# Optimization experiments

Hardware: AMD Instinct MI355X
Metric: run time of the kernel (lower is better)

The kernel has to match this reference:

```python
import jax, jax.numpy as jnp
import numpy as np

T, N, F, H = 64, 20000, 8, 32
E = 320000
NEG_SLOPE = 0.01  # torch.nn.LeakyReLU default


def setup_inputs() -> dict:
    key = jax.random.key(0)
    ks = jax.random.split(key, 16)
    g = lambda k, shape, fan_in: jax.random.normal(k, shape, jnp.float32) * (1.0 / np.sqrt(fan_in))
    return {
        "x": jax.random.normal(ks[0], (T, N, F), jnp.float32),
        "edge_index": jax.random.randint(ks[1], (2, E), 0, N, jnp.int64),
        "edge_weight": jax.random.uniform(ks[2], (E,), jnp.float32),
        "h": jnp.zeros((N, H), jnp.float32),
        # GConvGRU(K=1): each ChebConv reduces to a dense Linear (only T_0 = X term)
        "Wxz": g(ks[3], (F, H), F), "bxz": jnp.zeros((H,), jnp.float32),
        "Whz": g(ks[4], (H, H), H), "bhz": jnp.zeros((H,), jnp.float32),
        "Wxr": g(ks[5], (F, H), F), "bxr": jnp.zeros((H,), jnp.float32),
        "Whr": g(ks[6], (H, H), H), "bhr": jnp.zeros((H,), jnp.float32),
        "Wxh": g(ks[7], (F, H), F), "bxh": jnp.zeros((H,), jnp.float32),
        "Whh": g(ks[8], (H, H), H), "bhh": jnp.zeros((H,), jnp.float32),
        "W1": g(ks[9], (H, 1), H), "b1": jnp.zeros((1,), jnp.float32),
        "W2": g(ks[10], (N, 1), N), "b2": jnp.zeros((1,), jnp.float32),
    }


def reference(x, edge_index, edge_weight, h,
              Wxz, bxz, Whz, bhz, Wxr, bxr, Whr, bhr, Wxh, bxh, Whh, bhh,
              W1, b1, W2, b2):
    # GConvGRU with Chebyshev order K=1: each ChebConv is out = X @ W + b
    # (edge_index / edge_weight only participate for K >= 2, faithful to source).
    def gru_step(hc, xt):  # hc: [N,H], xt: [N,F]
        z = jax.nn.sigmoid(xt @ Wxz + bxz + hc @ Whz + bhz)
        r = jax.nn.sigmoid(xt @ Wxr + bxr + hc @ Whr + bhr)
        h_tilde = jnp.tanh(xt @ Wxh + bxh + (hc * r) @ Whh + bhh)
        hn = z * hc + (1.0 - z) * h_tilde
        return hn, hn

    h_fin, h_tensor = jax.lax.scan(gru_step, h, x)  # h_tensor: [T,N,H]
    a = jax.nn.leaky_relu(h_tensor, NEG_SLOPE)       # LeakyReLU(h_tensor)
    a = jax.nn.leaky_relu(a @ W1 + b1, NEG_SLOPE)    # linear1 -> [T,N,1], then LeakyReLU
    a = a[..., 0]                                    # squeeze -> [T,N]
    out = (a @ W2 + b2)[..., 0]                      # linear2 -> [T,1] -> squeeze -> [T]
    return (out, h_fin)
```

## Files before the change

kernel.cpp:

```cpp
#include <hip/hip_runtime.h>
#include <hip/hip_bf16.h>

#define T_STEPS 64
#define N_NODES 20000
#define F_IN    8
#define H_DIM   32
#define NEG_SLOPE 0.01f
#define WS_STRIDE 32
#define LOG2E 1.44269504f

typedef __attribute__((ext_vector_type(8))) short bf16x8;
typedef __attribute__((ext_vector_type(4))) float f32x4;

#define MFMA(a, b, c) __builtin_amdgcn_mfma_f32_16x16x32_bf16((a), (b), (c), 0, 0, 0)

__device__ __forceinline__ unsigned short f2bf(float f) {
    unsigned u = __float_as_uint(f);
    u += 0x7FFFu + ((u >> 16) & 1u);
    return (unsigned short)(u >> 16);
}
__device__ __forceinline__ float bf2f(unsigned short s) {
    return __uint_as_float(((unsigned)s) << 16);
}
__device__ __forceinline__ void split_pack8_rne(const float* v, bf16x8& hi, bf16x8& lo) {
    union { unsigned u[4]; bf16x8 v8; } H, L;
#pragma unroll
    for (int p = 0; p < 4; ++p) {
        float a = v[2*p], b = v[2*p+1];
        unsigned short ha = f2bf(a), hb = f2bf(b);
        unsigned short la = f2bf(a - bf2f(ha)), lb = f2bf(b - bf2f(hb));
        H.u[p] = (unsigned)ha | ((unsigned)hb << 16);
        L.u[p] = (unsigned)la | ((unsigned)lb << 16);
    }
    hi = H.v8; lo = L.v8;
}

__device__ __forceinline__ unsigned cvtpk(float a, float b) {
    union { __hip_bfloat162 h; unsigned u; } U;
    U.h = __float22bfloat162_rn(float2{a, b});
    return U.u;
}


__device__ __forceinline__ void load_wfragW(const float* __restrict__ W, int c, int q,
                                            int Rout, int Rown, int Roth, float scale,
                                            bf16x8& hi, bf16x8& lo) {
    float v[8];
#pragma unroll
    for (int j = 0; j < 8; ++j) {
        int dim = (j < 4) ? (Rown + 4*q + j) : (Roth + 4*q + (j - 4));
        v[j] = W[dim * H_DIM + (Rout + c)] * scale;
    }
    split_pack8_rne(v, hi, lo);
}

__device__ __forceinline__ bf16x8 load_xwfragW(const float* __restrict__ Wx,
                                               const float* __restrict__ bx,
                                               const float* __restrict__ bh,
                                               int c, int q, int Rout, float scale) {
    union { unsigned short s[8]; bf16x8 v8; } U;
#pragma unroll
    for (int j = 0; j < 8; ++j) U.s[j] = 0;
    if (q == 0) {
#pragma unroll
        for (int j = 0; j < 8; ++j) U.s[j] = f2bf(Wx[j * H_DIM + Rout + c] * scale);
    } else if (q == 1) {
#pragma unroll
        for (int j = 0; j < 8; ++j) {
            float w0 = Wx[j * H_DIM + Rout + c] * scale;
            unsigned short h = f2bf(w0);
            U.s[j] = f2bf(w0 - bf2f(h));
        }
    } else if (q == 3) {
        float b = (bx[Rout + c] + bh[Rout + c]) * scale;
        unsigned short h = f2bf(b);
        U.s[0] = h;
        U.s[1] = f2bf(b - bf2f(h));
    }
    return U.v8;
}

__device__ __forceinline__ bf16x8 build_xbfrag2(const float* v, int q) {
    union { unsigned u[4]; bf16x8 v8; } U;
#pragma unroll
    for (int p = 0; p < 4; ++p) {
        unsigned val = cvtpk(v[2*p], v[2*p+1]);
        if (q == 2) val = 0u;
        if (q == 3) val = (p == 0) ? 0x3F803F80u : 0u;
        U.u[p] = val;
    }
    return U.v8;
}

__device__ __forceinline__ bf16x8 frag_own(unsigned w01, unsigned w23) {
    union { unsigned u[4]; bf16x8 v8; } U;
    U.u[0] = w01; U.u[1] = w23; U.u[2] = 0u; U.u[3] = 0u;
    return U.v8;
}
__device__ __forceinline__ bf16x8 frag_peer(unsigned w01, unsigned w23) {
    union { unsigned u[4]; bf16x8 v8; } U;
    U.u[0] = 0u; U.u[1] = 0u; U.u[2] = w01; U.u[3] = w23;
    return U.v8;
}

__device__ __forceinline__ float sigmoid2_f(float xp) {
    return __builtin_amdgcn_rcpf(1.0f + __builtin_amdgcn_exp2f(-xp));
}
__device__ __forceinline__ float tanh2_f(float yp) {
    return 1.0f - 2.0f * __builtin_amdgcn_rcpf(1.0f + __builtin_amdgcn_exp2f(yp));
}
__device__ __forceinline__ float leaky_f(float x) {
    return fmaxf(x, NEG_SLOPE * x);
}

__global__ void final_kernel(const float* __restrict__ ws, const float* __restrict__ b2,
                             float* __restrict__ out) {
    int t = threadIdx.x;
    if (t < T_STEPS) out[t] = ws[t * WS_STRIDE] + b2[0];
}

__global__ __launch_bounds__(128, 3) void rgcn_mfma_kernel(
    const float* __restrict__ x,
    const float* __restrict__ h0,
    const float* __restrict__ Wxz, const float* __restrict__ bxz,
    const float* __restrict__ Whz, const float* __restrict__ bhz,
    const float* __restrict__ Wxr, const float* __restrict__ bxr,
    const float* __restrict__ Whr, const float* __restrict__ bhr,
    const float* __restrict__ Wxh, const float* __restrict__ bxh,
    const float* __restrict__ Whh, const float* __restrict__ bhh,
    const float* __restrict__ W1,  const float* __restrict__ b1,
    const float* __restrict__ W2,
    float* __restrict__ ws,
    float* __restrict__ out)
{
    const int tid  = threadIdx.x;
    const int w    = tid >> 6;
    const int l    = tid & 63;
    const int c    = l & 15;
    const int q    = l >> 4;
    const int base = blockIdx.x * 16;
    const int node = base + c;
    const int Rown = 16 * w;
    const int Roth = 16 - Rown;

    __shared__ __align__(8) uint2 hxbuf[2][2][4][16];
    __shared__ __align__(8) uint2 rhbuf[2][4][16];
    __shared__ unsigned short pbuf16[T_STEPS][130];

    bf16x8 WHrOh, WHrOl, WHzh, WHzl, WHhh, WHhl;
    load_wfragW(Whr, c, q, Rown, Rown, Roth, LOG2E,        WHrOh, WHrOl);
    load_wfragW(Whz, c, q, Rown, Rown, Roth, LOG2E,        WHzh,  WHzl);
    load_wfragW(Whh, c, q, Rown, Rown, Roth, 2.0f * LOG2E, WHhh,  WHhl);
    bf16x8 WXrO = load_xwfragW(Wxr, bxr, bhr, c, q, Rown, LOG2E);
    bf16x8 WXz  = load_xwfragW(Wxz, bxz, bhz, c, q, Rown, LOG2E);
    bf16x8 WXh  = load_xwfragW(Wxh, bxh, bhh, c, q, Rown, 2.0f * LOG2E);

    float w1v[4];
#pragma unroll
    for (int i = 0; i < 4; ++i) w1v[i] = W1[Rown + 4*q + i];
    const float b1s = b1[0];
    const float w2l = W2[node];

    float hv[4];
    unsigned own01, own23;
    {
        float4 h4 = ((const float4*)(h0 + (size_t)node * H_DIM + Rown))[q];
        hv[0] = h4.x; hv[1] = h4.y; hv[2] = h4.z; hv[3] = h4.w;
        own01 = cvtpk(hv[0], hv[1]);
        own23 = cvtpk(hv[2], hv[3]);
        hxbuf[0][w][q][c] = uint2{own01, own23};
    }

    const f32x4 zero4 = {0.0f, 0.0f, 0.0f, 0.0f};

    f32x4 axrO, axz, axh;
    {
        const float4* xp = (const float4*)(x + (size_t)node * F_IN);
        float4 x0 = xp[0], x1 = xp[1];
        float xv[8] = {x0.x, x0.y, x0.z, x0.w, x1.x, x1.y, x1.z, x1.w};
        bf16x8 fx0 = build_xbfrag2(xv, q);
        axrO = MFMA(WXrO, fx0, zero4);
        axz  = MFMA(WXz,  fx0, zero4);
        axh  = MFMA(WXh,  fx0, zero4);
    }
    float4 cx0, cx1;
    {
        const float4* xp = (const float4*)(x + (size_t)(N_NODES * F_IN)
                                             + (size_t)node * F_IN);
        cx0 = xp[0]; cx1 = xp[1];
    }

    __syncthreads();

#pragma unroll 1
    for (int t = 0; t < T_STEPS; ++t) {
        const int rp = t & 1;

        uint2 ohp = hxbuf[rp][1 - w][q][c];

        bf16x8 fhO = frag_own(own01, own23);
        f32x4 arA = MFMA(WHrOh, fhO, axrO);
        f32x4 arB = MFMA(WHrOl, fhO, zero4);
        f32x4 azA = MFMA(WHzh,  fhO, axz);
        f32x4 azB = MFMA(WHzl,  fhO, zero4);

        int tt = (t + 2 < T_STEPS) ? (t + 2) : (T_STEPS - 1);
        const float4* xp = (const float4*)(x + (size_t)tt * (N_NODES * F_IN)
                                             + (size_t)node * F_IN);
        float4 nx0 = xp[0], nx1 = xp[1];

        bf16x8 fhP = frag_peer(ohp.x, ohp.y);
        arA = MFMA(WHrOh, fhP, arA);
        arB = MFMA(WHrOl, fhP, arB);
        azA = MFMA(WHzh,  fhP, azA);
        azB = MFMA(WHzl,  fhP, azB);

        f32x4 arO = arA + arB;

        float rh4[4];
#pragma unroll
        for (int i = 0; i < 4; ++i) rh4[i] = sigmoid2_f(arO[i]) * hv[i];
        unsigned rh01 = cvtpk(rh4[0], rh4[1]);
        unsigned rh23 = cvtpk(rh4[2], rh4[3]);
        rhbuf[w][q][c] = uint2{rh01, rh23};

        bf16x8 frO = frag_own(rh01, rh23);
        f32x4 ahA = MFMA(WHhh, frO, axh);
        f32x4 ahB = MFMA(WHhl, frO, zero4);

        float nxv[8] = {cx0.x, cx0.y, cx0.z, cx0.w, cx1.x, cx1.y, cx1.z, cx1.w};
        bf16x8 fxn = build_xbfrag2(nxv, q);

        __syncthreads();

        uint2 orhp = rhbuf[1 - w][q][c];
        f32x4 nxrO = MFMA(WXrO, fxn, zero4);
        f32x4 nxz  = MFMA(WXz,  fxn, zero4);
        f32x4 nxh  = MFMA(WXh,  fxn, zero4);

        f32x4 az = azA + azB;
        float zv[4];
#pragma unroll
        for (int i = 0; i < 4; ++i) zv[i] = sigmoid2_f(az[i]);

        bf16x8 frP = frag_peer(orhp.x, orhp.y);
        ahA = MFMA(WHhh, frP, ahA);
        ahB = MFMA(WHhl, frP, ahB);
        f32x4 ah = ahA + ahB;

        float pnew = 0.0f;
#pragma unroll
        for (int i = 0; i < 4; ++i) {
            float th = tanh2_f(ah[i]);
            float hn = th + zv[i] * (hv[i] - th);
            hv[i] = hn;
            pnew = fmaf(leaky_f(hn), w1v[i], pnew);
        }
        pbuf16[t][tid] = (unsigned short)cvtpk(pnew, pnew);

        own01 = cvtpk(hv[0], hv[1]);
        own23 = cvtpk(hv[2], hv[3]);
        hxbuf[1 - rp][w][q][c] = uint2{own01, own23};

        axrO = nxrO; axz = nxz; axh = nxh;
        cx0 = nx0; cx1 = nx1;

        __syncthreads();
    }

#pragma unroll
    for (int rep = 0; rep < 8; ++rep) {
        int t = w * 32 + rep * 4 + q;
        float s = 0.0f;
#pragma unroll
        for (int g = 0; g < 8; ++g) s += bf2f(pbuf16[t][g * 16 + c]);
        float a2 = leaky_f(s + b1s) * w2l;
        a2 += __shfl_xor(a2, 1); a2 += __shfl_xor(a2, 2);
        a2 += __shfl_xor(a2, 4); a2 += __shfl_xor(a2, 8);
        if (c == 0) atomicAdd(&ws[t * WS_STRIDE], a2);
    }

    *(float4*)(out + T_STEPS + (size_t)node * H_DIM + Rown + 4*q) =
        (float4){hv[0], hv[1], hv[2], hv[3]};
}

extern "C" void kernel_launch(void* const* d_in, const int* in_sizes, int n_in,
                              void* d_out, int out_size, void* d_ws, size_t ws_size,
                              hipStream_t stream) {
    const float* x    = (const float*)d_in[0];
    const float* h0   = (const float*)d_in[3];
    const float* Wxz  = (const float*)d_in[4];
    const float* bxz  = (const float*)d_in[5];
    const float* Whz  = (const float*)d_in[6];
    const float* bhz  = (const float*)d_in[7];
    const float* Wxr  = (const float*)d_in[8];
    const float* bxr  = (const float*)d_in[9];
    const float* Whr  = (const float*)d_in[10];
    const float* bhr  = (const float*)d_in[11];
    const float* Wxh  = (const float*)d_in[12];
    const float* bxh  = (const float*)d_in[13];
    const float* Whh  = (const float*)d_in[14];
    const float* bhh  = (const float*)d_in[15];
    const float* W1   = (const float*)d_in[16];
    const float* b1   = (const float*)d_in[17];
    const float* W2   = (const float*)d_in[18];
    const float* b2   = (const float*)d_in[19];
    float* out = (float*)d_out;
    float* ws  = (float*)d_ws;

    const int grid = N_NODES / 16;
    rgcn_mfma_kernel<<<grid, 128, 0, stream>>>(
        x, h0, Wxz, bxz, Whz, bhz, Wxr, bxr, Whr, bhr,
        Wxh, bxh, Whh, bhh, W1, b1, W2, ws, out);

    final_kernel<<<1, 64, 0, stream>>>(ws, b2, out);
}
```

Measured before the change: 187.2 us.

## Prefetch block's x into LDS as bf16, merge own/peer MFMAs, reduce partials via shuffles

```diff
diff --git a/kernel.cpp b/kernel.cpp
--- a/kernel.cpp
+++ b/kernel.cpp
@@ -80,26 +80,10 @@
     return U.v8;
 }
 
-__device__ __forceinline__ bf16x8 build_xbfrag2(const float* v, int q) {
+__device__ __forceinline__ bf16x8 frag4(unsigned o01, unsigned o23,
+                                        unsigned p01, unsigned p23) {
     union { unsigned u[4]; bf16x8 v8; } U;
-#pragma unroll
-    for (int p = 0; p < 4; ++p) {
-        unsigned val = cvtpk(v[2*p], v[2*p+1]);
-        if (q == 2) val = 0u;
-        if (q == 3) val = (p == 0) ? 0x3F803F80u : 0u;
-        U.u[p] = val;
-    }
-    return U.v8;
-}
-
-__device__ __forceinline__ bf16x8 frag_own(unsigned w01, unsigned w23) {
-    union { unsigned u[4]; bf16x8 v8; } U;
-    U.u[0] = w01; U.u[1] = w23; U.u[2] = 0u; U.u[3] = 0u;
-    return U.v8;
-}
-__device__ __forceinline__ bf16x8 frag_peer(unsigned w01, unsigned w23) {
-    union { unsigned u[4]; bf16x8 v8; } U;
-    U.u[0] = 0u; U.u[1] = 0u; U.u[2] = w01; U.u[3] = w23;
+    U.u[0] = o01; U.u[1] = o23; U.u[2] = p01; U.u[3] = p23;
     return U.v8;
 }
 
@@ -143,17 +127,18 @@
     const int Rown = 16 * w;
     const int Roth = 16 - Rown;
 
+    __shared__ __align__(16) unsigned xbuf[T_STEPS][16][4];
     __shared__ __align__(8) uint2 hxbuf[2][2][4][16];
     __shared__ __align__(8) uint2 rhbuf[2][4][16];
-    __shared__ unsigned short pbuf16[T_STEPS][130];
-
-    bf16x8 WHrOh, WHrOl, WHzh, WHzl, WHhh, WHhl;
-    load_wfragW(Whr, c, q, Rown, Rown, Roth, LOG2E,        WHrOh, WHrOl);
-    load_wfragW(Whz, c, q, Rown, Rown, Roth, LOG2E,        WHzh,  WHzl);
-    load_wfragW(Whh, c, q, Rown, Rown, Roth, 2.0f * LOG2E, WHhh,  WHhl);
-    bf16x8 WXrO = load_xwfragW(Wxr, bxr, bhr, c, q, Rown, LOG2E);
-    bf16x8 WXz  = load_xwfragW(Wxz, bxz, bhz, c, q, Rown, LOG2E);
-    bf16x8 WXh  = load_xwfragW(Wxh, bxh, bhh, c, q, Rown, 2.0f * LOG2E);
+    __shared__ unsigned short pbuf16[T_STEPS][2][17];
+
+    bf16x8 WHrh, WHrl, WHzh, WHzl, WHhh, WHhl;
+    load_wfragW(Whr, c, q, Rown, Rown, Roth, LOG2E,        WHrh, WHrl);
+    load_wfragW(Whz, c, q, Rown, Rown, Roth, LOG2E,        WHzh, WHzl);
+    load_wfragW(Whh, c, q, Rown, Rown, Roth, 2.0f * LOG2E, WHhh, WHhl);
+    bf16x8 WXr = load_xwfragW(Wxr, bxr, bhr, c, q, Rown, LOG2E);
+    bf16x8 WXz = load_xwfragW(Wxz, bxz, bhz, c, q, Rown, LOG2E);
+    bf16x8 WXh = load_xwfragW(Wxh, bxh, bhh, c, q, Rown, 2.0f * LOG2E);
 
     float w1v[4];
 #pragma unroll
@@ -171,82 +156,72 @@
         hxbuf[0][w][q][c] = uint2{own01, own23};
     }
 
+#pragma unroll
+    for (int it = 0; it < 16; ++it) {
+        int idx = it * 128 + tid;
+        int t   = idx >> 5;
+        int ce  = (idx >> 1) & 15;
+        int hf  = idx & 1;
+        const float4 v = *(const float4*)(
+            x + ((size_t)t * N_NODES + base + ce) * F_IN + hf * 4);
+        xbuf[t][ce][hf * 2]     = cvtpk(v.x, v.y);
+        xbuf[t][ce][hf * 2 + 1] = cvtpk(v.z, v.w);
+    }
+
     const f32x4 zero4 = {0.0f, 0.0f, 0.0f, 0.0f};
-
-    f32x4 axrO, axz, axh;
+    const unsigned ONES2 = 0x3F803F80u;
+    const bool q3 = (q == 3);
+
+    __syncthreads();
+
+    f32x4 axr, axz, axh;
     {
-        const float4* xp = (const float4*)(x + (size_t)node * F_IN);
-        float4 x0 = xp[0], x1 = xp[1];
-        float xv[8] = {x0.x, x0.y, x0.z, x0.w, x1.x, x1.y, x1.z, x1.w};
-        bf16x8 fx0 = build_xbfrag2(xv, q);
-        axrO = MFMA(WXrO, fx0, zero4);
-        axz  = MFMA(WXz,  fx0, zero4);
-        axh  = MFMA(WXh,  fx0, zero4);
-    }
-    float4 cx0, cx1;
-    {
-        const float4* xp = (const float4*)(x + (size_t)(N_NODES * F_IN)
-                                             + (size_t)node * F_IN);
-        cx0 = xp[0]; cx1 = xp[1];
-    }
-
-    __syncthreads();
+        union { uint4 u4; } X; X.u4 = *(const uint4*)&xbuf[0][c][0];
+        bf16x8 fx0 = frag4(q3 ? ONES2 : X.u4.x, X.u4.y, X.u4.z, X.u4.w);
+        axr = MFMA(WXr, fx0, zero4);
+        axz = MFMA(WXz, fx0, zero4);
+        axh = MFMA(WXh, fx0, zero4);
+    }
 
 #pragma unroll 1
     for (int t = 0; t < T_STEPS; ++t) {
         const int rp = t & 1;
 
         uint2 ohp = hxbuf[rp][1 - w][q][c];
-
-        bf16x8 fhO = frag_own(own01, own23);
-        f32x4 arA = MFMA(WHrOh, fhO, axrO);
-        f32x4 arB = MFMA(WHrOl, fhO, zero4);
-        f32x4 azA = MFMA(WHzh,  fhO, axz);
-        f32x4 azB = MFMA(WHzl,  fhO, zero4);
-
-        int tt = (t + 2 < T_STEPS) ? (t + 2) : (T_STEPS - 1);
-        const float4* xp = (const float4*)(x + (size_t)tt * (N_NODES * F_IN)
-                                             + (size_t)node * F_IN);
-        float4 nx0 = xp[0], nx1 = xp[1];
-
-        bf16x8 fhP = frag_peer(ohp.x, ohp.y);
-        arA = MFMA(WHrOh, fhP, arA);
-        arB = MFMA(WHrOl, fhP, arB);
-        azA = MFMA(WHzh,  fhP, azA);
-        azB = MFMA(WHzl,  fhP, azB);
-
-        f32x4 arO = arA + arB;
+        bf16x8 fh = frag4(own01, own23, ohp.x, ohp.y);
+
+        f32x4 arA = MFMA(WHrh, fh, axr);
+        f32x4 arB = MFMA(WHrl, fh, zero4);
+        f32x4 az  = MFMA(WHzh, fh, axz);
+        az        = MFMA(WHzl, fh, az);
+        f32x4 ar  = arA + arB;
 
         float rh4[4];
 #pragma unroll
-        for (int i = 0; i < 4; ++i) rh4[i] = sigmoid2_f(arO[i]) * hv[i];
+        for (int i = 0; i < 4; ++i) rh4[i] = sigmoid2_f(ar[i]) * hv[i];
         unsigned rh01 = cvtpk(rh4[0], rh4[1]);
         unsigned rh23 = cvtpk(rh4[2], rh4[3]);
         rhbuf[w][q][c] = uint2{rh01, rh23};
 
-        bf16x8 frO = frag_own(rh01, rh23);
-        f32x4 ahA = MFMA(WHhh, frO, axh);
-        f32x4 ahB = MFMA(WHhl, frO, zero4);
-
-        float nxv[8] = {cx0.x, cx0.y, cx0.z, cx0.w, cx1.x, cx1.y, cx1.z, cx1.w};
-        bf16x8 fxn = build_xbfrag2(nxv, q);
-
         __syncthreads();
 
-        uint2 orhp = rhbuf[1 - w][q][c];
-        f32x4 nxrO = MFMA(WXrO, fxn, zero4);
-        f32x4 nxz  = MFMA(WXz,  fxn, zero4);
-        f32x4 nxh  = MFMA(WXh,  fxn, zero4);
-
-        f32x4 az = azA + azB;
+        int tt = (t + 1 < T_STEPS) ? (t + 1) : (T_STEPS - 1);
+        union { uint4 u4; } X; X.u4 = *(const uint4*)&xbuf[tt][c][0];
+        uint2 orh = rhbuf[1 - w][q][c];
+
+        bf16x8 fxn = frag4(q3 ? ONES2 : X.u4.x, X.u4.y, X.u4.z, X.u4.w);
+        f32x4 nxr = MFMA(WXr, fxn, zero4);
+        f32x4 nxz = MFMA(WXz, fxn, zero4);
+        f32x4 nxh = MFMA(WXh, fxn, zero4);
+
         float zv[4];
 #pragma unroll
         for (int i = 0; i < 4; ++i) zv[i] = sigmoid2_f(az[i]);
 
-        bf16x8 frP = frag_peer(orhp.x, orhp.y);
-        ahA = MFMA(WHhh, frP, ahA);
-        ahB = MFMA(WHhl, frP, ahB);
-        f32x4 ah = ahA + ahB;
+        bf16x8 fr = frag4(rh01, rh23, orh.x, orh.y);
+        f32x4 ahA = MFMA(WHhh, fr, axh);
+        f32x4 ahB = MFMA(WHhl, fr, zero4);
+        f32x4 ah  = ahA + ahB;
 
         float pnew = 0.0f;
 #pragma unroll
@@ -256,14 +231,15 @@
             hv[i] = hn;
             pnew = fmaf(leaky_f(hn), w1v[i], pnew);
         }
-        pbuf16[t][tid] = (unsigned short)cvtpk(pnew, pnew);
+        pnew += __shfl_xor(pnew, 16);
+        pnew += __shfl_xor(pnew, 32);
+        if (l < 16) pbuf16[t][w][c] = (unsigned short)cvtpk(pnew, pnew);
 
         own01 = cvtpk(hv[0], hv[1]);
         own23 = cvtpk(hv[2], hv[3]);
         hxbuf[1 - rp][w][q][c] = uint2{own01, own23};
 
-        axrO = nxrO; axz = nxz; axh = nxh;
-        cx0 = nx0; cx1 = nx1;
+        axr = nxr; axz = nxz; axh = nxh;
 
         __syncthreads();
     }
@@ -271,9 +247,7 @@
 #pragma unroll
     for (int rep = 0; rep < 8; ++rep) {
         int t = w * 32 + rep * 4 + q;
-        float s = 0.0f;
-#pragma unroll
-        for (int g = 0; g < 8; ++g) s += bf2f(pbuf16[t][g * 16 + c]);
+        float s = bf2f(pbuf16[t][0][c]) + bf2f(pbuf16[t][1][c]);
         float a2 = leaky_f(s + b1s) * w2l;
         a2 += __shfl_xor(a2, 1); a2 += __shfl_xor(a2, 2);
         a2 += __shfl_xor(a2, 4); a2 += __shfl_xor(a2, 8);
```

Measured after the change: 179.2 us. 4.3% less time.
